# Kernel optimization log

Measured on AMD Instinct MI355X. Metric: run time of the kernel, lower is better.

The kernel has to match this reference:

```python
import jax, jax.numpy as jnp
import numpy as np
from jax import lax

B, F, N = 1024, 512, 8  # batch, feature_dim, num_of_subAttention


def setup_inputs() -> dict:
    key = jax.random.key(0)
    ks = jax.random.split(key, 8)
    sc = 0.02
    return {
        "vx": jax.random.normal(ks[0], (B, F), dtype=jnp.float32),
        "ax": jax.random.normal(ks[1], (B, F), dtype=jnp.float32),
        # stacked per-unit MLP params (N units)
        "W1": jax.random.normal(ks[2], (N, F, 2 * F), dtype=jnp.float32) * sc,
        "b1": jnp.zeros((N, F), jnp.float32),
        "W2": jax.random.normal(ks[3], (N, F, F), dtype=jnp.float32) * sc,
        "b2": jnp.zeros((N, F), jnp.float32),
        # conv pipeline params (OIHW)
        "conv1_w": jax.random.normal(ks[4], (F, F, 3, 3), dtype=jnp.float32) * sc,
        "conv1_b": jnp.zeros((F,), jnp.float32),
        "conv2_w": jax.random.normal(ks[5], (F, F, 3, 3), dtype=jnp.float32) * sc,
        "conv2_b": jnp.zeros((F,), jnp.float32),
    }


def reference(vx, ax, W1, b1, W2, b2, conv1_w, conv1_b, conv2_w, conv2_b):
    # --- N AttentionUnits, vectorized over the unit axis n ---
    x = jnp.concatenate([vx, ax], axis=-1)                      # [B, 2F]
    # Dropout(0.5) is identity in eval mode.
    h = jax.nn.relu(jnp.einsum('bi,nfi->bnf', x, W1) + b1)      # [B, N, F]
    att = jax.nn.relu(jnp.einsum('bnf,ngf->bng', h, W2) + b2)   # [B, N, F]

    # vx broadcast over units, elementwise attention, then permute to [B, F, N]
    va = jnp.transpose(vx[:, None, :] * att, (0, 2, 1))         # [B, F, N]
    # rank-1 broadcast along trailing axis -> conv input [B, F, N, N]
    t = jnp.broadcast_to(va[..., None], (B, F, N, N))

    dn = ('NCHW', 'OIHW', 'NCHW')
    y = lax.conv_general_dilated(t, conv1_w, (1, 1), 'SAME', dimension_numbers=dn)
    y = y + conv1_b[None, :, None, None]
    k = N // 2
    y = lax.reduce_window(y, -jnp.inf, lax.max, (1, 1, k, k), (1, 1, k, k), 'VALID')  # [B,F,2,2]
    y = lax.conv_general_dilated(y, conv2_w, (1, 1), 'SAME', dimension_numbers=dn)
    y = y + conv2_b[None, :, None, None]
    y = jnp.mean(y, axis=(2, 3))                                # AdaptiveAvgPool2d((1,1)) -> [B, F]
    return jax.nn.relu(y)
```

## Files before the change

### kernel.cpp

```cpp
#include <hip/hip_runtime.h>
#include <hip/hip_bf16.h>


typedef __attribute__((ext_vector_type(8))) short short8;
typedef __attribute__((ext_vector_type(4))) float f32x4;

__device__ __forceinline__ void gload16(const void* g, void* l) {
    __builtin_amdgcn_global_load_lds(
        (const __attribute__((address_space(1))) void*)g,
        (__attribute__((address_space(3))) void*)l, 16, 0, 0);
}

template<int BM, int BN, bool RELU, bool BIAS, bool OUT_BF16>
__global__ __launch_bounds__(256) void gemm_mfma(
    const __hip_bfloat16* __restrict__ A, int lda, long sA,
    const __hip_bfloat16* __restrict__ B, int ldb, long sB,
    void* __restrict__ Cv, int ldc, long sC,
    const float* __restrict__ bias, long sBias,
    int K)
{
    constexpr int MI = BM / 32, NI = BN / 32;
    constexpr int GA = BM / 16, GB = BN / 16;
    constexpr int nA = (GA * 2) / 4, nB = (GB * 2) / 4;
    __shared__ __align__(16) char As[128 * BM];
    __shared__ __align__(16) char Bs[128 * BN];

    const int z = blockIdx.z;
    A += (long)z * sA;
    B += (long)z * sB;
    const int bm = blockIdx.y * BM;
    const int bn = blockIdx.x * BN;
    const int t = threadIdx.x, lane = t & 63, wid = t >> 6;
    const int q = lane >> 4, lr = lane & 15;
    const int wrow = (wid >> 1) * (BM / 2), wcol = (wid & 1) * (BN / 2);

    const int m_loc = lane >> 2;
    const int cst = ((lane & 3) - (m_loc >> 1)) & 3;
    const long abase = ((long)(bm + m_loc) * lda + cst * 8) * 2;
    const long bbase = ((long)(bn + m_loc) * ldb + cst * 8) * 2;
    const int ro = lr * 4;
    const int csel = (lr >> 1);

    f32x4 acc[MI][NI] = {};

    for (int k0 = 0; k0 < K; k0 += 64) {
        if (k0) __syncthreads();
        #pragma unroll
        for (int i = 0; i < nA; ++i) {
            int s = wid * nA + i, g = s % GA, h = s / GA;
            gload16((const char*)A + abase + ((long)g * 16 * lda + h * 32 + k0) * 2,
                    As + (h * (BM * 4) + g * 64) * 16);
        }
        #pragma unroll
        for (int i = 0; i < nB; ++i) {
            int s = wid * nB + i, g = s % GB, h = s / GB;
            gload16((const char*)B + bbase + ((long)g * 16 * ldb + h * 32 + k0) * 2,
                    Bs + (h * (BN * 4) + g * 64) * 16);
        }
        __syncthreads();

        #pragma unroll
        for (int ks = 0; ks < 2; ++ks) {
            short8 af[MI], bf[NI];
            #pragma unroll
            for (int mi = 0; mi < MI; ++mi) {
                int u = ks * (BM * 4) + ((wrow >> 4) + mi) * 64 + ro + ((q + csel) & 3);
                af[mi] = *(const short8*)(As + u * 16);
            }
            #pragma unroll
            for (int ni = 0; ni < NI; ++ni) {
                int u = ks * (BN * 4) + ((wcol >> 4) + ni) * 64 + ro + ((q + csel) & 3);
                bf[ni] = *(const short8*)(Bs + u * 16);
            }
            #pragma unroll
            for (int mi = 0; mi < MI; ++mi)
                #pragma unroll
                for (int ni = 0; ni < NI; ++ni)
                    acc[mi][ni] = __builtin_amdgcn_mfma_f32_16x16x32_bf16(
                        af[mi], bf[ni], acc[mi][ni], 0, 0, 0);
        }
    }

    #pragma unroll
    for (int mi = 0; mi < MI; ++mi) {
        #pragma unroll
        for (int ni = 0; ni < NI; ++ni) {
            int gn = bn + wcol + ni * 16 + lr;
            float bv = 0.f;
            if constexpr (BIAS) bv = bias[z * sBias + gn];
            #pragma unroll
            for (int r = 0; r < 4; ++r) {
                long gm = bm + wrow + mi * 16 + q * 4 + r;
                float v = acc[mi][ni][r] + bv;
                if constexpr (RELU) v = fmaxf(v, 0.f);
                if constexpr (OUT_BF16)
                    ((__hip_bfloat16*)Cv)[z * sC + gm * ldc + gn] = __float2bfloat16(v);
                else
                    ((float*)Cv)[z * sC + gm * ldc + gn] = v;
            }
        }
    }
}

__global__ __launch_bounds__(256) void conv_gemm_pool(
    const float* __restrict__ vx,
    const __hip_bfloat16* __restrict__ att,
    const __hip_bfloat16* __restrict__ B,
    float* __restrict__ PM)
{
    constexpr int BM = 128, BN = 128, MI = 4, NI = 4;
    constexpr int GB = 8, nB = 4;
    const int ldb = 1536;
    __shared__ __align__(16) char As[128 * BM];
    __shared__ __align__(16) char Bs[128 * BN];

    const int bm = blockIdx.x * BM;
    const int bn = blockIdx.y * BN;
    const int t = threadIdx.x, lane = t & 63, wid = t >> 6;
    const int q = lane >> 4, lr = lane & 15;
    const int wrow = (wid >> 1) * 64, wcol = (wid & 1) * 64;

    const int m_loc = lane >> 2;
    const int cstB = ((lane & 3) - (m_loc >> 1)) & 3;
    const long bbase = ((long)(bn + m_loc) * ldb + cstB * 8) * 2;
    const int ro = lr * 4;
    const int csel = (lr >> 1);

    int lh[4], lrow[4], lkc[4];
    #pragma unroll
    for (int u = 0; u < 4; ++u) {
        int l = t + u * 256;
        lh[u]   = l >> 9;
        int r16 = (l >> 2) & 15;
        lrow[u] = ((l >> 6) & 7) * 16 + r16;
        lkc[u]  = ((l & 3) - (r16 >> 1)) & 3;
    }

    f32x4 acc[MI][NI] = {};

    for (int kk = 0; kk < 24; ++kk) {
        const int ki = kk >> 3;
        const int c0 = (kk & 7) << 6;
        const int k0 = kk << 6;
        if (kk) __syncthreads();
        #pragma unroll
        for (int i = 0; i < nB; ++i) {
            int s = wid * nB + i, g = s % GB, h = s / GB;
            gload16((const char*)B + bbase + ((long)g * 16 * ldb + h * 32 + k0) * 2,
                    Bs + (h * (BN * 4) + g * 64) * 16);
        }
        #pragma unroll
        for (int u = 0; u < 4; ++u) {
            int l = t + u * 256;
            int gm = bm + lrow[u];
            int b = gm >> 3, ii = gm & 7;
            int ip = ii + ki - 1;
            int c = c0 + lh[u] * 32 + lkc[u] * 8;
            short8 val = {0, 0, 0, 0, 0, 0, 0, 0};
            if (ip >= 0 && ip < 8) {
                short8 a8 = *(const short8*)(att + (((long)b << 12) + (ip << 9) + c));
                const float* vp = vx + (b << 9) + c;
                float4 v0 = *(const float4*)vp;
                float4 v1 = *(const float4*)(vp + 4);
                float vf[8] = {v0.x, v0.y, v0.z, v0.w, v1.x, v1.y, v1.z, v1.w};
                #pragma unroll
                for (int j = 0; j < 8; ++j) {
                    union { short s; __hip_bfloat16 h; } ua; ua.s = a8[j];
                    union { __hip_bfloat16 h; short s; } ub;
                    ub.h = __float2bfloat16(__bfloat162float(ua.h) * vf[j]);
                    val[j] = ub.s;
                }
            }
            *(short8*)(As + l * 16) = val;
        }
        __syncthreads();

        #pragma unroll
        for (int ks = 0; ks < 2; ++ks) {
            short8 af[MI], bf[NI];
            #pragma unroll
            for (int mi = 0; mi < MI; ++mi) {
                int u = ks * (BM * 4) + ((wrow >> 4) + mi) * 64 + ro + ((q + csel) & 3);
                af[mi] = *(const short8*)(As + u * 16);
            }
            #pragma unroll
            for (int ni = 0; ni < NI; ++ni) {
                int u = ks * (BN * 4) + ((wcol >> 4) + ni) * 64 + ro + ((q + csel) & 3);
                bf[ni] = *(const short8*)(Bs + u * 16);
            }
            #pragma unroll
            for (int mi = 0; mi < MI; ++mi)
                #pragma unroll
                for (int ni = 0; ni < NI; ++ni)
                    acc[mi][ni] = __builtin_amdgcn_mfma_f32_16x16x32_bf16(
                        af[mi], bf[ni], acc[mi][ni], 0, 0, 0);
        }
    }

    #pragma unroll
    for (int mi = 0; mi < MI; ++mi) {
        int rowbase = bm + wrow + mi * 16;
        int batch = (rowbase >> 3) + (q >> 1);
        int pi = q & 1;
        #pragma unroll
        for (int ni = 0; ni < NI; ++ni) {
            int gn = bn + wcol + ni * 16 + lr;
            int v = gn >> 9, o = gn & 511;
            float m = fmaxf(fmaxf(acc[mi][ni][0], acc[mi][ni][1]),
                            fmaxf(acc[mi][ni][2], acc[mi][ni][3]));
            PM[((long)v * 1024 + batch) * 1024 + pi * 512 + o] = m;
        }
    }
}

__global__ __launch_bounds__(256) void prep_kernel(
    const float* __restrict__ vx, const float* __restrict__ ax,
    const float* __restrict__ W1, const float* __restrict__ W2,
    const float* __restrict__ c1w, const float* __restrict__ c2w,
    __hip_bfloat16* __restrict__ X,  __hip_bfloat16* __restrict__ W1b,
    __hip_bfloat16* __restrict__ W2b, __hip_bfloat16* __restrict__ WC,
    __hip_bfloat16* __restrict__ M2)
{
    int blk = blockIdx.x, t = threadIdx.x;
    if (blk < 2048) {
        int i = blk * 256 + t, b = i >> 9, c = i & 511;
        X[((long)b << 10) + c]       = __float2bfloat16(vx[i]);
        X[((long)b << 10) + 512 + c] = __float2bfloat16(ax[i]);
    } else if (blk < 8192) {
        int j = (blk - 2048) * 256 + t;
        const float* src = (j < 1048576) ? W1 : W2;
        __hip_bfloat16* dst = (j < 1048576) ? W1b : W2b;
        int k = (j < 1048576) ? j : j - 1048576;
        float4 v = ((const float4*)src)[k];
        union { __hip_bfloat16 h[4]; short4 s; } u;
        u.h[0] = __float2bfloat16(v.x); u.h[1] = __float2bfloat16(v.y);
        u.h[2] = __float2bfloat16(v.z); u.h[3] = __float2bfloat16(v.w);
        ((short4*)dst)[k] = u.s;
    } else if (blk < 17408) {
        int b2 = blk - 8192;
        int row = b2 / 6, col = (b2 % 6) * 256 + t;
        int v = row >> 9, o = row & 511;
        int ki = col >> 9, c = col & 511;
        const float* w = c1w + ((long)(o * 512 + c) * 3 + ki) * 3;
        float s = w[1];
        if (v != 0) s += w[0];
        if (v != 2) s += w[2];
        WC[(long)row * 1536 + col] = __float2bfloat16(s);
    } else {
        int b2 = blk - 17408;
        int o2 = b2 >> 3, col = (b2 & 7) * 256 + t;
        int c = col >> 2, pi = (col >> 1) & 1, pj = col & 1;
        const float* w = c2w + (long)(o2 * 512 + c) * 9;
        float s = w[pi * 3 + pj] + w[pi * 3 + pj + 1]
                + w[(pi + 1) * 3 + pj] + w[(pi + 1) * 3 + pj + 1];
        M2[(long)o2 * 2048 + col] = __float2bfloat16(0.25f * s);
    }
}

__global__ __launch_bounds__(256) void combine_kernel(
    const float* __restrict__ PM, const float* __restrict__ c1b,
    __hip_bfloat16* __restrict__ P)
{
    int idx = blockIdx.x * 256 + threadIdx.x;
    int b = idx >> 9, o = idx & 511;
    float bias = c1b[o];
    const long vs = 1024L * 1024;
    long base = (long)b * 1024 + o;
    float l0 = PM[base],            l1 = PM[base + 512];
    float m0 = PM[vs + base],       m1 = PM[vs + base + 512];
    float r0 = PM[2 * vs + base],   r1 = PM[2 * vs + base + 512];
    union { __hip_bfloat16 h[4]; short4 s; } u;
    u.h[0] = __float2bfloat16(fmaxf(l0, m0) + bias);
    u.h[1] = __float2bfloat16(fmaxf(m0, r0) + bias);
    u.h[2] = __float2bfloat16(fmaxf(l1, m1) + bias);
    u.h[3] = __float2bfloat16(fmaxf(m1, r1) + bias);
    ((short4*)(P + (long)b * 2048 + o * 4))[0] = u.s;
}

extern "C" void kernel_launch(void* const* d_in, const int* in_sizes, int n_in,
                              void* d_out, int out_size, void* d_ws, size_t ws_size,
                              hipStream_t stream)
{
    const float* vx  = (const float*)d_in[0];
    const float* ax  = (const float*)d_in[1];
    const float* W1  = (const float*)d_in[2];
    const float* b1  = (const float*)d_in[3];
    const float* W2  = (const float*)d_in[4];
    const float* b2  = (const float*)d_in[5];
    const float* c1w = (const float*)d_in[6];
    const float* c1b = (const float*)d_in[7];
    const float* c2w = (const float*)d_in[8];
    const float* c2b = (const float*)d_in[9];
    float* out = (float*)d_out;
    char* w = (char*)d_ws;

    const long MiB = 1 << 20;
    __hip_bfloat16* Xbf   = (__hip_bfloat16*)(w + 0 * MiB);
    __hip_bfloat16* W1bf  = (__hip_bfloat16*)(w + 2 * MiB);
    __hip_bfloat16* Hbf   = (__hip_bfloat16*)(w + 10 * MiB);
    __hip_bfloat16* W2bf  = (__hip_bfloat16*)(w + 18 * MiB);
    __hip_bfloat16* ATTbf = (__hip_bfloat16*)(w + 22 * MiB);
    __hip_bfloat16* WCbf  = (__hip_bfloat16*)(w + 30 * MiB);
    float*          PM    = (float*)         (w + 35 * MiB);
    __hip_bfloat16* Pbf   = (__hip_bfloat16*)(w + 47 * MiB);
    __hip_bfloat16* M2bf  = (__hip_bfloat16*)(w + 51 * MiB);

    prep_kernel<<<21504, 256, 0, stream>>>(vx, ax, W1, W2, c1w, c2w,
                                           Xbf, W1bf, W2bf, WCbf, M2bf);

    gemm_mfma<128, 128, true, true, true><<<dim3(32, 8, 1), 256, 0, stream>>>(
        Xbf, 1024, 0, W1bf, 1024, 0, Hbf, 4096, 0, b1, 0, 1024);

    gemm_mfma<128, 128, true, true, true><<<dim3(4, 8, 8), 256, 0, stream>>>(
        Hbf, 4096, 512, W2bf, 512, 262144, ATTbf, 4096, 512, b2, 512, 512);

    conv_gemm_pool<<<dim3(64, 12), 256, 0, stream>>>(vx, ATTbf, WCbf, PM);

    combine_kernel<<<2048, 256, 0, stream>>>(PM, c1b, Pbf);

    gemm_mfma<64, 64, true, true, false><<<dim3(8, 16, 1), 256, 0, stream>>>(
        Pbf, 2048, 0, M2bf, 2048, 0, out, 512, 0, c2b, 0, 2048);
}
```

Before: 224.1 us.

## Reuse staged vx*att tile across the three conv taps via padded LDS layout

Reorders the K loop so the three kernel-row taps for each 64-channel chunk run consecutively. The elementwise vx*att product is built into LDS only once per chunk, in a padded layout with zero rows at each batch boundary, and the shifted tap rows are read directly from it. This removes two of every three global loads and bf16 conversions of the A operand. The LDS buffer grows, the per-row padding stride may cause bank conflicts, and the B-operand indexing is changed to match the new loop order.

```diff
diff --git a/kernel.cpp b/kernel.cpp
--- a/kernel.cpp
+++ b/kernel.cpp
@@ -111,7 +111,7 @@
     constexpr int BM = 128, BN = 128, MI = 4, NI = 4;
     constexpr int GB = 8, nB = 4;
     const int ldb = 1536;
-    __shared__ __align__(16) char As[128 * BM];
+    __shared__ __align__(16) char VAs[160 * 144];
     __shared__ __align__(16) char Bs[128 * BN];
 
     const int bm = blockIdx.x * BM;
@@ -126,43 +126,46 @@
     const int ro = lr * 4;
     const int csel = (lr >> 1);
 
-    int lh[4], lrow[4], lkc[4];
+    {
+        int b = t >> 4, side = (t >> 3) & 1, w8 = t & 7;
+        int pr = b * 10 + side * 9;
+        short8 z8 = {0, 0, 0, 0, 0, 0, 0, 0};
+        *(short8*)(VAs + (pr * 9 + w8) * 16) = z8;
+    }
+
+    int abase_[MI];
     #pragma unroll
-    for (int u = 0; u < 4; ++u) {
-        int l = t + u * 256;
-        lh[u]   = l >> 9;
-        int r16 = (l >> 2) & 15;
-        lrow[u] = ((l >> 6) & 7) * 16 + r16;
-        lkc[u]  = ((l & 3) - (r16 >> 1)) & 3;
+    for (int mi = 0; mi < MI; ++mi) {
+        int m = wrow + mi * 16 + lr;
+        abase_[mi] = (((m >> 3) * 10 + (m & 7)) * 9 + q) * 16;
     }
 
     f32x4 acc[MI][NI] = {};
 
     for (int kk = 0; kk < 24; ++kk) {
-        const int ki = kk >> 3;
-        const int c0 = (kk & 7) << 6;
-        const int k0 = kk << 6;
+        const int ki = kk - (kk / 3) * 3;
+        const int c0 = (kk / 3) << 6;
+        const int k0B = ki * 512 + c0;
         if (kk) __syncthreads();
         #pragma unroll
         for (int i = 0; i < nB; ++i) {
             int s = wid * nB + i, g = s % GB, h = s / GB;
-            gload16((const char*)B + bbase + ((long)g * 16 * ldb + h * 32 + k0) * 2,
+            gload16((const char*)B + bbase + ((long)g * 16 * ldb + k0B + h * 32) * 2,
                     Bs + (h * (BN * 4) + g * 64) * 16);
         }
-        #pragma unroll
-        for (int u = 0; u < 4; ++u) {
-            int l = t + u * 256;
-            int gm = bm + lrow[u];
-            int b = gm >> 3, ii = gm & 7;
-            int ip = ii + ki - 1;
-            int c = c0 + lh[u] * 32 + lkc[u] * 8;
-            short8 val = {0, 0, 0, 0, 0, 0, 0, 0};
-            if (ip >= 0 && ip < 8) {
-                short8 a8 = *(const short8*)(att + (((long)b << 12) + (ip << 9) + c));
-                const float* vp = vx + (b << 9) + c;
+        if (ki == 0) {
+            #pragma unroll
+            for (int u = 0; u < 4; ++u) {
+                int li = t + u * 256;
+                int r = li >> 3, w8 = li & 7;
+                int gm = bm + r;
+                int c = c0 + w8 * 8;
+                short8 a8 = *(const short8*)(att + (long)gm * 512 + c);
+                const float* vp = vx + ((gm >> 3) << 9) + c;
                 float4 v0 = *(const float4*)vp;
                 float4 v1 = *(const float4*)(vp + 4);
                 float vf[8] = {v0.x, v0.y, v0.z, v0.w, v1.x, v1.y, v1.z, v1.w};
+                short8 val;
                 #pragma unroll
                 for (int j = 0; j < 8; ++j) {
                     union { short s; __hip_bfloat16 h; } ua; ua.s = a8[j];
@@ -170,8 +173,9 @@
                     ub.h = __float2bfloat16(__bfloat162float(ua.h) * vf[j]);
                     val[j] = ub.s;
                 }
-            }
-            *(short8*)(As + l * 16) = val;
+                int pr = (r >> 3) * 10 + 1 + (r & 7);
+                *(short8*)(VAs + (pr * 9 + w8) * 16) = val;
+            }
         }
         __syncthreads();
 
@@ -179,10 +183,8 @@
         for (int ks = 0; ks < 2; ++ks) {
             short8 af[MI], bf[NI];
             #pragma unroll
-            for (int mi = 0; mi < MI; ++mi) {
-                int u = ks * (BM * 4) + ((wrow >> 4) + mi) * 64 + ro + ((q + csel) & 3);
-                af[mi] = *(const short8*)(As + u * 16);
-            }
+            for (int mi = 0; mi < MI; ++mi)
+                af[mi] = *(const short8*)(VAs + abase_[mi] + ki * 144 + ks * 64);
             #pragma unroll
             for (int ni = 0; ni < NI; ++ni) {
                 int u = ks * (BN * 4) + ((wcol >> 4) + ni) * 64 + ro + ((q + csel) & 3);
```

New measurement: 208.9 us. 1.07x faster.
